# Optimization experiments

Hardware: AMD Instinct MI355X
Metric: run time of the kernel (lower is better)

## Reference

```python
import jax, jax.numpy as jnp
import numpy as np

H = 16          # num_heads
HD = 64         # head_dim = latent_dim // num_heads
RHD = 32        # rope_head_dim = head_dim // 2
NHD = 32        # nope_head_dim
Q_LAT = 256     # latent_dim // compression_ratio
KV_LAT = 204    # xf_latent_dim // (compression_ratio + 1)
MAX_LEN = 2048
THETA = 10000.0
EPS = 1e-5


def _rope_tables():
    half = RHD // 2  # 16
    freqs = 1.0 / THETA ** (np.arange(half, dtype=np.float32) / half)
    t = np.arange(MAX_LEN, dtype=np.float32)
    ang = np.outer(t, freqs)  # (MAX_LEN, half)
    return jnp.asarray(np.cos(ang)), jnp.asarray(np.sin(ang))

COS, SIN = _rope_tables()


def _ln(x, g, b):
    m = jnp.mean(x, axis=-1, keepdims=True)
    v = jnp.var(x, axis=-1, keepdims=True)
    return (x - m) * jax.lax.rsqrt(v + EPS) * g + b


def _rope(t, cos, sin):
    # t: (..., L, RHD); cos/sin: (L, RHD//2); interleaved even/odd convention
    ev, od = t[..., 0::2], t[..., 1::2]
    oe = ev * cos - od * sin
    oo = ev * sin + od * cos
    return jnp.stack([oe, oo], axis=-1).reshape(t.shape)


def setup_inputs() -> dict:
    key = jax.random.key(0)
    ks = jax.random.split(key, 12)
    D = 1024
    s = 0.02
    return {
        "x": jax.random.normal(ks[0], (2, 2048, D), jnp.float32),
        "xf": jax.random.normal(ks[1], (2, 2048, D), jnp.float32),
        "Wqc": jax.random.normal(ks[2], (D, Q_LAT), jnp.float32) * s,
        "gq": jnp.ones((Q_LAT,), jnp.float32),
        "bq": jnp.zeros((Q_LAT,), jnp.float32),
        "Wq_rope": jax.random.normal(ks[3], (Q_LAT, H * RHD), jnp.float32) * s,
        "Wq_nope": jax.random.normal(ks[4], (Q_LAT, H * NHD), jnp.float32) * s,
        "Wkvc": jax.random.normal(ks[5], (D, KV_LAT), jnp.float32) * s,
        "gkv": jnp.ones((KV_LAT,), jnp.float32),
        "bkv": jnp.zeros((KV_LAT,), jnp.float32),
        "Wk_nope": jax.random.normal(ks[6], (KV_LAT, H * NHD), jnp.float32) * s,
        "Wv": jax.random.normal(ks[7], (KV_LAT, H * HD), jnp.float32) * s,
        "Wkr": jax.random.normal(ks[8], (D, RHD), jnp.float32) * s,
        "Wo": jax.random.normal(ks[9], (D, D), jnp.float32) * s,
        "bo": jnp.zeros((D,), jnp.float32),
    }


def reference(x, xf, Wqc, gq, bq, Wq_rope, Wq_nope, Wkvc, gkv, bkv, Wk_nope, Wv, Wkr, Wo, bo):
    B, T, D = x.shape
    S = xf.shape[1]

    # query path: compress -> LN -> decoupled decompress
    ql = _ln(x @ Wqc, gq, bq)                                   # (B,T,Q_LAT)
    q_nope = (ql @ Wq_nope).reshape(B, T, H, NHD).transpose(0, 2, 1, 3)  # (B,H,T,NHD)
    q_rope = (ql @ Wq_rope).reshape(B, T, H, RHD).transpose(0, 2, 1, 3)  # (B,H,T,RHD)

    # key/value path: compress -> LN -> decompress; shared single rope head
    kvl = _ln(xf @ Wkvc, gkv, bkv)                              # (B,S,KV_LAT)
    k_nope = (kvl @ Wk_nope).reshape(B, S, H, NHD).transpose(0, 2, 1, 3)  # (B,H,S,NHD)
    v = (kvl @ Wv).reshape(B, S, H, HD).transpose(0, 2, 1, 3)   # (B,H,S,HD)
    k_rope = (xf @ Wkr).reshape(B, S, 1, RHD).transpose(0, 2, 1, 3)       # (B,1,S,RHD)

    q_rope = _rope(q_rope, COS[:T], SIN[:T])
    k_rope = _rope(k_rope, COS[:S], SIN[:S]) / H
    k_rope = jnp.broadcast_to(k_rope, (B, H, S, RHD))

    q = jnp.concatenate([q_nope, q_rope], axis=-1)              # (B,H,T,HD)
    k = jnp.concatenate([k_nope, k_rope], axis=-1)              # (B,H,S,HD)

    scale = 1.0 / jnp.sqrt(jnp.asarray(HD, q.dtype))
    scores = jnp.einsum("bhtd,bhsd->bhts", q, k) * scale
    attn = jax.nn.softmax(scores, axis=-1)
    o = jnp.einsum("bhts,bhsd->bhtd", attn, v)                  # (B,H,T,HD)
    o = o.transpose(0, 2, 1, 3).reshape(B, T, H * HD)
    return o @ Wo + bo
```

## Files before the change

### kernel.cpp

```cpp
#include <hip/hip_runtime.h>
#include <hip/hip_bf16.h>
#include <math.h>

#define SEQ 2048

typedef __bf16 bf16x8 __attribute__((ext_vector_type(8)));
typedef float  f32x4  __attribute__((ext_vector_type(4)));

#if __has_builtin(__builtin_amdgcn_exp2f)
#define EXP2(x) __builtin_amdgcn_exp2f(x)
#else
#define EXP2(x) exp2f(x)
#endif

__device__ __forceinline__ unsigned short f2bf(float f) {
  __bf16 h = (__bf16)f;
  return __builtin_bit_cast(unsigned short, h);
}

__device__ __forceinline__ void gload16(const unsigned short* g, unsigned short* l) {
  __builtin_amdgcn_global_load_lds(
      (const __attribute__((address_space(1))) void*)g,
      (__attribute__((address_space(3))) void*)l, 16, 0, 0);
}

__device__ __forceinline__ unsigned cvtpk(float lo, float hi) {
  unsigned r;
  asm("v_cvt_pk_bf16_f32 %0, %1, %2" : "=v"(r) : "v"(lo), "v"(hi));
  return r;
}
__device__ __forceinline__ void plswap32(unsigned &a, unsigned &b) {
  asm("v_permlane32_swap_b32 %0, %1" : "+v"(a), "+v"(b));
}
__device__ __forceinline__ void plswap16(unsigned &a, unsigned &b) {
  asm("v_permlane16_swap_b32 %0, %1" : "+v"(a), "+v"(b));
}

#define CLOG (0.125f * 1.44269504f)

struct WPrep {
  const float* src[8];
  unsigned short* dst[8];
  int K[8], N[8], NR[8], KC[8], nb[8];
  float2* cst;
  const float* xs[2];
  unsigned short* xd[2];
};

__global__ __launch_bounds__(256) void wprep_kernel(WPrep p)
{
  __shared__ float tile[32][33];
  int bid = blockIdx.x;
  if (bid < 128) {
    const int idx = bid * 256 + threadIdx.x;
    const int pos = idx >> 4, i = idx & 15;
    const float freq = EXP2(-(float)i * 0.8304820237f);
    const float ang = (float)pos * freq;
    p.cst[idx] = make_float2(cosf(ang), sinf(ang));
    return;
  }
  bid -= 128;
  if (bid < 4096) {
    const int sel = bid >> 11;
    const long base = (long)(bid & 2047) * 2048 + threadIdx.x * 8;
    const float4 a = *(const float4*)&p.xs[sel][base];
    const float4 b = *(const float4*)&p.xs[sel][base + 4];
    ushort4 u0, u1;
    u0.x = f2bf(a.x); u0.y = f2bf(a.y); u0.z = f2bf(a.z); u0.w = f2bf(a.w);
    u1.x = f2bf(b.x); u1.y = f2bf(b.y); u1.z = f2bf(b.z); u1.w = f2bf(b.w);
    *(ushort4*)&p.xd[sel][base] = u0;
    *(ushort4*)&p.xd[sel][base + 4] = u1;
    return;
  }
  bid -= 4096;
  int di = 0;
  while (bid >= p.nb[di]) { bid -= p.nb[di]; ++di; }
  const float* src = p.src[di];
  unsigned short* dst = p.dst[di];
  const int K = p.K[di], N = p.N[di], KC = p.KC[di];
  const int nkx = KC >> 5;
  const int k0 = (bid % nkx) * 32, n0 = (bid / nkx) * 32;
  const int tx = threadIdx.x & 31, ty = threadIdx.x >> 5;
  for (int r = ty; r < 32; r += 8) {
    const int k = k0 + r, n = n0 + tx;
    tile[r][tx] = (k < K && n < N) ? src[(long)k * N + n] : 0.0f;
  }
  __syncthreads();
  for (int r = ty; r < 32; r += 8) {
    const int n = n0 + r, k = k0 + tx;
    dst[(long)n * KC + k] = f2bf(tile[tx][r]);
  }
}

template <int EPI, bool AF32>
__device__ __forceinline__ void gemm_body(
    unsigned short* smem,
    const void* __restrict__ Av, const unsigned short* __restrict__ BT,
    const float* __restrict__ bias, const float2* __restrict__ cst,
    void* __restrict__ C0v, void* __restrict__ C1v, int K, int N,
    int bx, int by)
{
  unsigned short* As = smem;
  unsigned short* Bs = smem + 2 * 128 * 32;
  const int tid = threadIdx.x;
  const int w = tid >> 6, lane = tid & 63;
  const int ln16 = lane & 15, quad = lane >> 4;
  const int wm = (w >> 1) * 64, wn = (w & 1) * 64;
  const int m0 = by * 128, n0 = bx * 128;
  const int rr = tid >> 2, cc = (tid & 3) * 8;

  const unsigned short* A = (const unsigned short*)Av;

  auto stageB = [&](int ib, int k0) {
    gload16(&BT[(long)(n0 + rr)      * K + k0 + cc], &Bs[ib * 4096 + rr * 32 + cc]);
    gload16(&BT[(long)(n0 + 64 + rr) * K + k0 + cc], &Bs[ib * 4096 + (64 + rr) * 32 + cc]);
  };
  auto stageAbf = [&](int ib, int k0) {
    gload16(&A[(long)(m0 + rr)      * K + k0 + cc], &As[ib * 4096 + rr * 32 + cc]);
    gload16(&A[(long)(m0 + 64 + rr) * K + k0 + cc], &As[ib * 4096 + (64 + rr) * 32 + cc]);
  };

  f32x4 acc[4][4];
#pragma unroll
  for (int i = 0; i < 4; ++i)
#pragma unroll
    for (int j = 0; j < 4; ++j)
#pragma unroll
      for (int r = 0; r < 4; ++r) acc[i][j][r] = 0.0f;

  stageB(0, 0);
  stageAbf(0, 0);

  int ib = 0;
  for (int k0 = 0; k0 < K; k0 += 32, ib ^= 1) {
    __syncthreads();
    const int kn = k0 + 32;
    if (kn < K) { stageB(ib ^ 1, kn); stageAbf(ib ^ 1, kn); }
    bf16x8 fa[4], fb[4];
#pragma unroll
    for (int i = 0; i < 4; ++i) fa[i] = *(const bf16x8*)&As[ib * 4096 + (wm + i * 16 + ln16) * 32 + quad * 8];
#pragma unroll
    for (int j = 0; j < 4; ++j) fb[j] = *(const bf16x8*)&Bs[ib * 4096 + (wn + j * 16 + ln16) * 32 + quad * 8];
#pragma unroll
    for (int i = 0; i < 4; ++i)
#pragma unroll
      for (int j = 0; j < 4; ++j)
        acc[i][j] = __builtin_amdgcn_mfma_f32_16x16x32_bf16(fa[i], fb[j], acc[i][j], 0, 0, 0);
  }

  if (EPI == 5 && n0 >= 512) {
    __syncthreads();
#pragma unroll
    for (int i = 0; i < 4; ++i) {
      const int rl = wm + i * 16 + quad * 4;
#pragma unroll
      for (int j = 0; j < 4; ++j) {
        const int cl = wn + j * 16 + ln16;
        ushort4 u;
        u.x = f2bf(acc[i][j][0]); u.y = f2bf(acc[i][j][1]);
        u.z = f2bf(acc[i][j][2]); u.w = f2bf(acc[i][j][3]);
        *(ushort4*)&smem[cl * 132 + rl] = u;
      }
    }
    __syncthreads();
    unsigned short* vT = (unsigned short*)C1v;
    const int b = m0 >> 11, sbase = m0 & (SEQ - 1);
    for (int q = tid; q < 128 * 16; q += 256) {
      const int cl = q >> 4, sch = (q & 15) * 8;
      bf16x8 val = *(const bf16x8*)&smem[cl * 132 + sch];
      const int c = (n0 - 512) + cl;
      const int hh = c >> 6, dd = c & 63;
      *(bf16x8*)&vT[((long)(b * 16 + hh) * 64 + dd) * SEQ + sbase + sch] = val;
    }
    return;
  }
#pragma unroll
  for (int i = 0; i < 4; ++i) {
    const int row0 = m0 + wm + i * 16 + quad * 4;
#pragma unroll
    for (int j = 0; j < 4; ++j) {
      const int col = n0 + wn + j * 16 + ln16;
      if (EPI == 3) {
        if (n0 < 512) {
          unsigned short* qn = (unsigned short*)C0v;
#pragma unroll
          for (int r = 0; r < 4; ++r) qn[(long)(row0 + r) * 512 + col] = f2bf(acc[i][j][r] * CLOG);
        } else {
          unsigned short* qr = (unsigned short*)C1v;
          const int c = col - 512;
          const int d = c & 31;
#pragma unroll
          for (int r = 0; r < 4; ++r) {
            const float v = acc[i][j][r];
            const float p = __shfl_xor(v, 1);
            const float2 t = cst[((row0 + r) & (SEQ - 1)) * 16 + (d >> 1)];
            const float o = ((d & 1) == 0) ? (v * t.x - p * t.y) : (p * t.y + v * t.x);
            qr[(long)(row0 + r) * 512 + c] = f2bf(o * CLOG);
          }
        }
      } else if (EPI == 5) {
        unsigned short* kn = (unsigned short*)C0v;
#pragma unroll
        for (int r = 0; r < 4; ++r) kn[(long)(row0 + r) * 512 + col] = f2bf(acc[i][j][r]);
      }
    }
  }
}

template <int E0, bool AF0, int E1, bool AF1>
__global__ __launch_bounds__(256) void gemm_dual1d(
    const void* __restrict__ A0, const unsigned short* __restrict__ BT0,
    void* __restrict__ C00, void* __restrict__ C01, int K0, int N0, int nx0, int nb0,
    const void* __restrict__ A1, const unsigned short* __restrict__ BT1,
    void* __restrict__ C10, void* __restrict__ C11, int K1, int N1, int nx1,
    const float2* __restrict__ cst)
{
  __shared__ unsigned short smem[16896];
  int bid = blockIdx.x;
  if (bid < nb0) {
    gemm_body<E0, AF0>(smem, A0, BT0, nullptr, cst, C00, C01, K0, N0, bid % nx0, bid / nx0);
  } else {
    bid -= nb0;
    gemm_body<E1, AF1>(smem, A1, BT1, nullptr, cst, C10, C11, K1, N1, bid % nx1, bid / nx1);
  }
}

template <int EPI>
__device__ __forceinline__ void gemm_wbody(
    unsigned short* smem,
    const unsigned short* __restrict__ A, const unsigned short* __restrict__ BT,
    const float* __restrict__ bias, const float2* __restrict__ cst,
    void* __restrict__ C0v, void* __restrict__ C1v, int K, int N,
    int bx, int by)
{
  unsigned short* As = smem;
  unsigned short* Bs = smem + 4096;
  const int tid = threadIdx.x;
  const int w = tid >> 6, lane = tid & 63;
  const int ln16 = lane & 15, quad = lane >> 4;
  const int wm = (w >> 1) * 32, wn = (w & 1) * 64;
  const int m0 = by * 64, n0 = bx * 128;
  const int rr = tid >> 2, cc = (tid & 3) * 8;

  auto stageA = [&](int ib, int k0) {
    gload16(&A[(long)(m0 + rr) * K + k0 + cc], &As[ib * 2048 + rr * 32 + cc]);
  };
  auto stageB = [&](int ib, int k0) {
    gload16(&BT[(long)(n0 + rr)      * K + k0 + cc], &Bs[ib * 4096 + rr * 32 + cc]);
    gload16(&BT[(long)(n0 + 64 + rr) * K + k0 + cc], &Bs[ib * 4096 + (64 + rr) * 32 + cc]);
  };

  f32x4 acc[2][4];
#pragma unroll
  for (int i = 0; i < 2; ++i)
#pragma unroll
    for (int j = 0; j < 4; ++j)
#pragma unroll
      for (int r = 0; r < 4; ++r) acc[i][j][r] = 0.0f;

  stageA(0, 0);
  stageB(0, 0);

  int ib = 0;
  for (int k0 = 0; k0 < K; k0 += 32, ib ^= 1) {
    __syncthreads();
    const int kn = k0 + 32;
    if (kn < K) { stageA(ib ^ 1, kn); stageB(ib ^ 1, kn); }
    bf16x8 fa[2], fb[4];
#pragma unroll
    for (int i = 0; i < 2; ++i) fa[i] = *(const bf16x8*)&As[ib * 2048 + (wm + i * 16 + ln16) * 32 + quad * 8];
#pragma unroll
    for (int j = 0; j < 4; ++j) fb[j] = *(const bf16x8*)&Bs[ib * 4096 + (wn + j * 16 + ln16) * 32 + quad * 8];
#pragma unroll
    for (int i = 0; i < 2; ++i)
#pragma unroll
      for (int j = 0; j < 4; ++j)
        acc[i][j] = __builtin_amdgcn_mfma_f32_16x16x32_bf16(fa[i], fb[j], acc[i][j], 0, 0, 0);
  }

#pragma unroll
  for (int i = 0; i < 2; ++i) {
    const int row0 = m0 + wm + i * 16 + quad * 4;
#pragma unroll
    for (int j = 0; j < 4; ++j) {
      const int col = n0 + wn + j * 16 + ln16;
      if (EPI == 0 || EPI == 1) {
        float* C = (float*)C0v;
        const float bv = (EPI == 1) ? bias[col] : 0.0f;
#pragma unroll
        for (int r = 0; r < 4; ++r) C[(long)(row0 + r) * N + col] = acc[i][j][r] + bv;
      } else if (EPI == 4) {
        if (col < 256) {
          float* kvl = (float*)C0v;
#pragma unroll
          for (int r = 0; r < 4; ++r) kvl[(long)(row0 + r) * 256 + col] = acc[i][j][r];
        } else if (col < 288) {
          unsigned short* kr = (unsigned short*)C1v;
          const int d = col - 256;
#pragma unroll
          for (int r = 0; r < 4; ++r) {
            const float v = acc[i][j][r];
            const float p = __shfl_xor(v, 1);
            const float2 t = cst[((row0 + r) & (SEQ - 1)) * 16 + (d >> 1)];
            const float o = ((d & 1) == 0) ? (v * t.x - p * t.y) : (p * t.y + v * t.x);
            kr[(long)(row0 + r) * 32 + d] = f2bf(o * 0.0625f);
          }
        }
      }
    }
  }
}

template <int EPI>
__global__ __launch_bounds__(256) void gemm_widek(
    const unsigned short* __restrict__ A, const unsigned short* __restrict__ BT,
    const float* __restrict__ bias, const float2* __restrict__ cst,
    void* __restrict__ C0, void* __restrict__ C1, int K, int N)
{
  __shared__ unsigned short smem[12288];
  gemm_wbody<EPI>(smem, A, BT, bias, cst, C0, C1, K, N, blockIdx.x, blockIdx.y);
}

template <int E0, int E1>
__global__ __launch_bounds__(256) void gemm_dualw1d(
    const unsigned short* __restrict__ A0, const unsigned short* __restrict__ BT0,
    void* __restrict__ C00, void* __restrict__ C01, int K0, int N0, int nx0, int nb0,
    const unsigned short* __restrict__ A1, const unsigned short* __restrict__ BT1,
    void* __restrict__ C10, void* __restrict__ C11, int K1, int N1, int nx1,
    const float2* __restrict__ cst)
{
  __shared__ unsigned short smem[12288];
  int bid = blockIdx.x;
  if (bid < nb0) {
    gemm_wbody<E0>(smem, A0, BT0, nullptr, cst, C00, C01, K0, N0, bid % nx0, bid / nx0);
  } else {
    bid -= nb0;
    gemm_wbody<E1>(smem, A1, BT1, nullptr, cst, C10, C11, K1, N1, bid % nx1, bid / nx1);
  }
}

__global__ __launch_bounds__(256) void ln_fast_kernel(
    const float* __restrict__ Xq, const float* __restrict__ Xkv,
    const float* __restrict__ gq, const float* __restrict__ bq,
    const float* __restrict__ gkv, const float* __restrict__ bkv,
    unsigned short* __restrict__ Yq, unsigned short* __restrict__ Ykv)
{
  const int tid = threadIdx.x;
  const int wv = tid >> 6, lane = tid & 63;
  const int row0 = blockIdx.x * 4 + wv;
  const bool isq = row0 < 4096;
  const int row = isq ? row0 : row0 - 4096;
  const float* X = isq ? Xq : Xkv;
  const float* g = isq ? gq : gkv;
  const float* b = isq ? bq : bkv;
  unsigned short* Y = isq ? Yq : Ykv;
  const int C = isq ? 256 : 204;
  const int Cp = isq ? 256 : 224;
  const int col = lane * 4;
  const bool valid = col < C;
  float4 v = make_float4(0.f, 0.f, 0.f, 0.f);
  if (valid) v = *(const float4*)&X[(long)row * 256 + col];
  float s1 = v.x + v.y + v.z + v.w;
  float s2 = v.x * v.x + v.y * v.y + v.z * v.z + v.w * v.w;
#pragma unroll
  for (int off = 1; off < 64; off <<= 1) {
    s1 += __shfl_xor(s1, off);
    s2 += __shfl_xor(s2, off);
  }
  const float mean = s1 / C;
  const float var  = s2 / C - mean * mean;
  const float rs = rsqrtf(var + 1e-5f);
  if (valid) {
    const float4 gv = *(const float4*)&g[col];
    const float4 bv = *(const float4*)&b[col];
    ushort4 u;
    u.x = f2bf((v.x - mean) * rs * gv.x + bv.x);
    u.y = f2bf((v.y - mean) * rs * gv.y + bv.y);
    u.z = f2bf((v.z - mean) * rs * gv.z + bv.z);
    u.w = f2bf((v.w - mean) * rs * gv.w + bv.w);
    *(ushort4*)&Y[(long)row * Cp + col] = u;
  } else if (col < Cp) {
    *(ushort4*)&Y[(long)row * Cp + col] = make_ushort4(0, 0, 0, 0);
  }
}

#define KSTR 36
#define VSTR 68
__global__ __launch_bounds__(256, 2) void attn_mfma_kernel(
    const unsigned short* __restrict__ qn, const unsigned short* __restrict__ qr,
    const unsigned short* __restrict__ kn, const unsigned short* __restrict__ kr,
    const unsigned short* __restrict__ vT, unsigned short* __restrict__ ob)
{
  __shared__ unsigned short Kn[2][64 * KSTR];
  __shared__ unsigned short Vs[2][64 * VSTR];
  const int id = blockIdx.x;
  const int xcd = id & 7, j = id >> 3;
  const int bh = xcd * 4 + (j & 3);
  const int tile = j >> 2;
  const int b = bh >> 4, h = bh & 15;
  const int t0 = tile * 128;
  const int tid = threadIdx.x;
  const int w = tid >> 6, lane = tid & 63;
  const int ln16 = lane & 15, quad = lane >> 4;
  const int trow = w * 16;
  const long bT = (long)b * SEQ;

  const int krow = tid >> 2, kc8 = (tid & 3) * 8;
  const int vd0 = tid >> 3, vc0 = (tid & 7) * 8;
  const int vd1 = vd0 + 32;

  bf16x8 q0A = *(const bf16x8*)&qn[(bT + t0 + trow + ln16) * 512 + h * 32 + quad * 8];
  bf16x8 q1A = *(const bf16x8*)&qr[(bT + t0 + trow + ln16) * 512 + h * 32 + quad * 8];
  bf16x8 q0B = *(const bf16x8*)&qn[(bT + t0 + 64 + trow + ln16) * 512 + h * 32 + quad * 8];
  bf16x8 q1B = *(const bf16x8*)&qr[(bT + t0 + 64 + trow + ln16) * 512 + h * 32 + quad * 8];

  auto loadKV = [&](int s0, bf16x8& rk0, bf16x8& rv0, bf16x8& rv1) {
    rk0 = *(const bf16x8*)&kn[(bT + s0 + krow) * 512 + h * 32 + kc8];
    rv0 = *(const bf16x8*)&vT[((long)bh * 64 + vd0) * SEQ + s0 + vc0];
    rv1 = *(const bf16x8*)&vT[((long)bh * 64 + vd1) * SEQ + s0 + vc0];
  };
  auto writeKV = [&](int ib, bf16x8 rk0, bf16x8 rv0, bf16x8 rv1) {
    *(bf16x8*)&Kn[ib][krow * KSTR + kc8] = rk0;
    *(bf16x8*)&Vs[ib][vd0 * VSTR + vc0] = rv0;
    *(bf16x8*)&Vs[ib][vd1 * VSTR + vc0] = rv1;
  };
  auto loadKrF = [&](int s0, bf16x8* f) {
#pragma unroll
    for (int nt = 0; nt < 4; ++nt)
      f[nt] = *(const bf16x8*)&kr[(bT + s0 + nt * 16 + ln16) * 32 + quad * 8];
  };
  auto pxform = [&](const f32x4* sf, float& l_part, bf16x8& a0, bf16x8& a1) {
    float p[16];
#pragma unroll
    for (int nt = 0; nt < 4; ++nt)
#pragma unroll
      for (int r = 0; r < 4; ++r) {
        const float e = EXP2(sf[nt][r]);
        p[nt * 4 + r] = e;
        l_part += e;
      }
    unsigned u0 = cvtpk(p[0],  p[1]),  u1 = cvtpk(p[2],  p[3]);
    unsigned u2 = cvtpk(p[4],  p[5]),  u3 = cvtpk(p[6],  p[7]);
    unsigned u4 = cvtpk(p[8],  p[9]),  u5 = cvtpk(p[10], p[11]);
    unsigned u6 = cvtpk(p[12], p[13]), u7 = cvtpk(p[14], p[15]);
    plswap32(u0, u2); plswap16(u0, u2);
    plswap32(u1, u3); plswap16(u1, u3);
    plswap32(u4, u6); plswap16(u4, u6);
    plswap32(u5, u7); plswap16(u5, u7);
    const uint4 w0 = make_uint4(u0, u1, u2, u3);
    const uint4 w1 = make_uint4(u4, u5, u6, u7);
    a0 = __builtin_bit_cast(bf16x8, w0);
    a1 = __builtin_bit_cast(bf16x8, w1);
  };

  bf16x8 ck0, cv0, cv1;
  bf16x8 nk0, nv0, nv1;
  bf16x8 ckr[4];
  loadKV(0, ck0, cv0, cv1);
  writeKV(0, ck0, cv0, cv1);
  loadKV(64, nk0, nv0, nv1);
  loadKrF(0, ckr);

  f32x4 o_acc[2][4];
#pragma unroll
  for (int g = 0; g < 2; ++g)
#pragma unroll
    for (int nt = 0; nt < 4; ++nt)
#pragma unroll
      for (int r = 0; r < 4; ++r) o_acc[g][nt][r] = 0.0f;
  float l_part[2] = {0.0f, 0.0f};

  int ib = 0;
  for (int s0 = 0; s0 < SEQ; s0 += 64, ib ^= 1) {
    __syncthreads();
    if (s0 + 64 < SEQ) {
      writeKV(ib ^ 1, nk0, nv0, nv1);
      if (s0 + 128 < SEQ) loadKV(s0 + 128, nk0, nv0, nv1);
    }

    bf16x8 ka[4];
#pragma unroll
    for (int nt = 0; nt < 4; ++nt)
      ka[nt] = *(const bf16x8*)&Kn[ib][(nt * 16 + ln16) * KSTR + quad * 8];

    f32x4 sfA[4], sfB[4];
#pragma unroll
    for (int nt = 0; nt < 4; ++nt)
#pragma unroll
      for (int r = 0; r < 4; ++r) { sfA[nt][r] = 0.0f; sfB[nt][r] = 0.0f; }
#pragma unroll
    for (int nt = 0; nt < 4; ++nt) {
      sfA[nt] = __builtin_amdgcn_mfma_f32_16x16x32_bf16(ka[nt], q0A, sfA[nt], 0, 0, 0);
      sfA[nt] = __builtin_amdgcn_mfma_f32_16x16x32_bf16(ckr[nt], q1A, sfA[nt], 0, 0, 0);
    }
#pragma unroll
    for (int nt = 0; nt < 4; ++nt) {
      sfB[nt] = __builtin_amdgcn_mfma_f32_16x16x32_bf16(ka[nt], q0B, sfB[nt], 0, 0, 0);
      sfB[nt] = __builtin_amdgcn_mfma_f32_16x16x32_bf16(ckr[nt], q1B, sfB[nt], 0, 0, 0);
    }

    if (s0 + 64 < SEQ) loadKrF(s0 + 64, ckr);

    bf16x8 a0A, a1A, a0B, a1B;
    pxform(sfA, l_part[0], a0A, a1A);
    pxform(sfB, l_part[1], a0B, a1B);

#pragma unroll
    for (int nt = 0; nt < 4; ++nt) {
      bf16x8 v0 = *(const bf16x8*)&Vs[ib][(nt * 16 + ln16) * VSTR + quad * 8];
      o_acc[0][nt] = __builtin_amdgcn_mfma_f32_16x16x32_bf16(a0A, v0, o_acc[0][nt], 0, 0, 0);
      o_acc[1][nt] = __builtin_amdgcn_mfma_f32_16x16x32_bf16(a0B, v0, o_acc[1][nt], 0, 0, 0);
      bf16x8 v1 = *(const bf16x8*)&Vs[ib][(nt * 16 + ln16) * VSTR + 32 + quad * 8];
      o_acc[0][nt] = __builtin_amdgcn_mfma_f32_16x16x32_bf16(a1A, v1, o_acc[0][nt], 0, 0, 0);
      o_acc[1][nt] = __builtin_amdgcn_mfma_f32_16x16x32_bf16(a1B, v1, o_acc[1][nt], 0, 0, 0);
    }
  }

#pragma unroll
  for (int g = 0; g < 2; ++g) {
    float l_i = l_part[g];
    l_i += __shfl_xor(l_i, 16);
    l_i += __shfl_xor(l_i, 32);
    const float lr = 1.0f / l_i;
    float lq[4];
#pragma unroll
    for (int r = 0; r < 4; ++r) lq[r] = __shfl(lr, quad * 4 + r);
#pragma unroll
    for (int r = 0; r < 4; ++r) {
      const long t = t0 + g * 64 + trow + quad * 4 + r;
      const long base = (bT + t) * 1024 + h * 64 + ln16;
#pragma unroll
      for (int nt = 0; nt < 4; ++nt)
        ob[base + nt * 16] = f2bf(o_acc[g][nt][r] * lq[r]);
    }
  }
}

extern "C" void kernel_launch(void* const* d_in, const int* in_sizes, int n_in,
                              void* d_out, int out_size, void* d_ws, size_t ws_size,
                              hipStream_t stream) {
  const float* x       = (const float*)d_in[0];
  const float* xf      = (const float*)d_in[1];
  const float* Wqc     = (const float*)d_in[2];
  const float* gq      = (const float*)d_in[3];
  const float* bq      = (const float*)d_in[4];
  const float* Wq_rope = (const float*)d_in[5];
  const float* Wq_nope = (const float*)d_in[6];
  const float* Wkvc    = (const float*)d_in[7];
  const float* gkv     = (const float*)d_in[8];
  const float* bkv     = (const float*)d_in[9];
  const float* Wk_nope = (const float*)d_in[10];
  const float* Wv      = (const float*)d_in[11];
  const float* Wkr     = (const float*)d_in[12];
  const float* Wo      = (const float*)d_in[13];
  const float* bo      = (const float*)d_in[14];
  float* out = (float*)d_out;

  const long R = 4096;
  float* ws = (float*)d_ws;
  float* ql_f  = ws;
  float* kvl_f = ql_f + R * 256;
  float2* cst  = (float2*)(kvl_f + R * 256);
  unsigned short* us = (unsigned short*)(cst + 2048 * 16);
  unsigned short* ql_bf  = us;  us += R * 256;
  unsigned short* kvl_bf = us;  us += R * 224;
  unsigned short* qn_bf  = us;  us += R * 512;
  unsigned short* qr_bf  = us;  us += R * 512;
  unsigned short* kn_bf  = us;  us += R * 512;
  unsigned short* kr_bf  = us;  us += R * 32;
  unsigned short* vT_bf  = us;  us += R * 1024;
  unsigned short* o_bf   = us;  us += R * 1024;
  unsigned short* x_bf   = us;  us += R * 1024;
  unsigned short* xf_bf  = us;  us += R * 1024;
  unsigned short* WqcT   = us;  us += 256 * 1024;
  unsigned short* WkvkrT = us;  us += 384 * 1024;
  unsigned short* WqnqrT = us;  us += 1024 * 256;
  unsigned short* WknvT  = us;  us += 1536 * 224;
  unsigned short* WoT    = us;  us += 1024 * 1024;

  WPrep p;
  const float* srcs[8] = {Wqc, Wkvc, Wkr, Wq_nope, Wq_rope, Wk_nope, Wv, Wo};
  unsigned short* dsts[8] = {WqcT, WkvkrT, WkvkrT + 256 * 1024,
                             WqnqrT, WqnqrT + 512 * 256,
                             WknvT, WknvT + 512 * 224, WoT};
  const int Ks[8]  = {1024, 1024, 1024, 256, 256, 204, 204, 1024};
  const int Ns[8]  = {256, 204, 32, 512, 512, 512, 1024, 1024};
  const int NRs[8] = {256, 256, 128, 512, 512, 512, 1024, 1024};
  const int KCs[8] = {1024, 1024, 1024, 256, 256, 224, 224, 1024};
  int total = 128 + 4096;
  for (int i = 0; i < 8; ++i) {
    p.src[i] = srcs[i]; p.dst[i] = dsts[i];
    p.K[i] = Ks[i]; p.N[i] = Ns[i]; p.NR[i] = NRs[i]; p.KC[i] = KCs[i];
    p.nb[i] = (KCs[i] / 32) * (NRs[i] / 32);
    total += p.nb[i];
  }
  p.cst = cst;
  p.xs[0] = x;  p.xs[1] = xf;
  p.xd[0] = x_bf; p.xd[1] = xf_bf;
  wprep_kernel<<<total, 256, 0, stream>>>(p);

  gemm_dualw1d<0, 4><<<320, 256, 0, stream>>>(
      x_bf, WqcT, ql_f, nullptr, 1024, 256, 2, 128,
      xf_bf, WkvkrT, kvl_f, kr_bf, 1024, 384, 3, cst);
  ln_fast_kernel<<<2048, 256, 0, stream>>>(ql_f, kvl_f, gq, bq, gkv, bkv, ql_bf, kvl_bf);
  gemm_dual1d<3, false, 5, false><<<640, 256, 0, stream>>>(
      ql_bf, WqnqrT, qn_bf, qr_bf, 256, 1024, 8, 256,
      kvl_bf, WknvT, kn_bf, vT_bf, 224, 1536, 12, cst);
  attn_mfma_kernel<<<512, 256, 0, stream>>>(qn_bf, qr_bf, kn_bf, kr_bf, vT_bf, o_bf);
  gemm_widek<1><<<dim3(8, 64), 256, 0, stream>>>(o_bf, WoT, bo, cst, out, nullptr, 1024, 1024);
}
```

Before: 208.3 us.

## Enlarge attention block to 256 query rows with 8 waves sharing K/V tiles

The attention kernel now runs 512 threads per block and covers 256 query rows, up from 256 threads and 128 rows, so the grid shrinks to 256 blocks. Each K/V tile staged in shared memory is reused by 8 waves instead of 4. This halves the global and LDS staging traffic per query row, and K/V loading is spread over more threads. In exchange, each barrier now waits on twice as many waves, and there is one block per CU instead of two, so less independent work can hide stalls.

```diff
diff --git a/kernel.cpp b/kernel.cpp
--- a/kernel.cpp
+++ b/kernel.cpp
@@ -386,7 +386,7 @@
 
 #define KSTR 36
 #define VSTR 68
-__global__ __launch_bounds__(256, 2) void attn_mfma_kernel(
+__global__ __launch_bounds__(512, 1) void attn_mfma_kernel(
     const unsigned short* __restrict__ qn, const unsigned short* __restrict__ qr,
     const unsigned short* __restrict__ kn, const unsigned short* __restrict__ kr,
     const unsigned short* __restrict__ vT, unsigned short* __restrict__ ob)
@@ -398,31 +398,28 @@
   const int bh = xcd * 4 + (j & 3);
   const int tile = j >> 2;
   const int b = bh >> 4, h = bh & 15;
-  const int t0 = tile * 128;
+  const int t0 = tile * 256;
   const int tid = threadIdx.x;
   const int w = tid >> 6, lane = tid & 63;
   const int ln16 = lane & 15, quad = lane >> 4;
   const int trow = w * 16;
   const long bT = (long)b * SEQ;
 
+  const int vdr = tid >> 3, vcc = (tid & 7) * 8;
   const int krow = tid >> 2, kc8 = (tid & 3) * 8;
-  const int vd0 = tid >> 3, vc0 = (tid & 7) * 8;
-  const int vd1 = vd0 + 32;
 
   bf16x8 q0A = *(const bf16x8*)&qn[(bT + t0 + trow + ln16) * 512 + h * 32 + quad * 8];
   bf16x8 q1A = *(const bf16x8*)&qr[(bT + t0 + trow + ln16) * 512 + h * 32 + quad * 8];
-  bf16x8 q0B = *(const bf16x8*)&qn[(bT + t0 + 64 + trow + ln16) * 512 + h * 32 + quad * 8];
-  bf16x8 q1B = *(const bf16x8*)&qr[(bT + t0 + 64 + trow + ln16) * 512 + h * 32 + quad * 8];
-
-  auto loadKV = [&](int s0, bf16x8& rk0, bf16x8& rv0, bf16x8& rv1) {
-    rk0 = *(const bf16x8*)&kn[(bT + s0 + krow) * 512 + h * 32 + kc8];
-    rv0 = *(const bf16x8*)&vT[((long)bh * 64 + vd0) * SEQ + s0 + vc0];
-    rv1 = *(const bf16x8*)&vT[((long)bh * 64 + vd1) * SEQ + s0 + vc0];
-  };
-  auto writeKV = [&](int ib, bf16x8 rk0, bf16x8 rv0, bf16x8 rv1) {
-    *(bf16x8*)&Kn[ib][krow * KSTR + kc8] = rk0;
-    *(bf16x8*)&Vs[ib][vd0 * VSTR + vc0] = rv0;
-    *(bf16x8*)&Vs[ib][vd1 * VSTR + vc0] = rv1;
+  bf16x8 q0B = *(const bf16x8*)&qn[(bT + t0 + 128 + trow + ln16) * 512 + h * 32 + quad * 8];
+  bf16x8 q1B = *(const bf16x8*)&qr[(bT + t0 + 128 + trow + ln16) * 512 + h * 32 + quad * 8];
+
+  auto loadKV = [&](int s0, bf16x8& rk, bf16x8& rv) {
+    rv = *(const bf16x8*)&vT[((long)bh * 64 + vdr) * SEQ + s0 + vcc];
+    if (tid < 256) rk = *(const bf16x8*)&kn[(bT + s0 + krow) * 512 + h * 32 + kc8];
+  };
+  auto writeKV = [&](int ib, bf16x8 rk, bf16x8 rv) {
+    *(bf16x8*)&Vs[ib][vdr * VSTR + vcc] = rv;
+    if (tid < 256) *(bf16x8*)&Kn[ib][krow * KSTR + kc8] = rk;
   };
   auto loadKrF = [&](int s0, bf16x8* f) {
 #pragma unroll
@@ -453,12 +450,12 @@
     a1 = __builtin_bit_cast(bf16x8, w1);
   };
 
-  bf16x8 ck0, cv0, cv1;
-  bf16x8 nk0, nv0, nv1;
+  bf16x8 ck, cv;
+  bf16x8 nk, nv;
   bf16x8 ckr[4];
-  loadKV(0, ck0, cv0, cv1);
-  writeKV(0, ck0, cv0, cv1);
-  loadKV(64, nk0, nv0, nv1);
+  loadKV(0, ck, cv);
+  writeKV(0, ck, cv);
+  loadKV(64, nk, nv);
   loadKrF(0, ckr);
 
   f32x4 o_acc[2][4];
@@ -474,8 +471,8 @@
   for (int s0 = 0; s0 < SEQ; s0 += 64, ib ^= 1) {
     __syncthreads();
     if (s0 + 64 < SEQ) {
-      writeKV(ib ^ 1, nk0, nv0, nv1);
-      if (s0 + 128 < SEQ) loadKV(s0 + 128, nk0, nv0, nv1);
+      writeKV(ib ^ 1, nk, nv);
+      if (s0 + 128 < SEQ) loadKV(s0 + 128, nk, nv);
     }
 
     bf16x8 ka[4];
@@ -527,7 +524,7 @@
     for (int r = 0; r < 4; ++r) lq[r] = __shfl(lr, quad * 4 + r);
 #pragma unroll
     for (int r = 0; r < 4; ++r) {
-      const long t = t0 + g * 64 + trow + quad * 4 + r;
+      const long t = t0 + g * 128 + trow + quad * 4 + r;
       const long base = (bT + t) * 1024 + h * 64 + ln16;
 #pragma unroll
       for (int nt = 0; nt < 4; ++nt)
@@ -606,6 +603,6 @@
   gemm_dual1d<3, false, 5, false><<<640, 256, 0, stream>>>(
       ql_bf, WqnqrT, qn_bf, qr_bf, 256, 1024, 8, 256,
       kvl_bf, WknvT, kn_bf, vT_bf, 224, 1536, 12, cst);
-  attn_mfma_kernel<<<512, 256, 0, stream>>>(qn_bf, qr_bf, kn_bf, kr_bf, vT_bf, o_bf);
+  attn_mfma_kernel<<<256, 512, 0, stream>>>(qn_bf, qr_bf, kn_bf, kr_bf, vT_bf, o_bf);
   gemm_widek<1><<<dim3(8, 64), 256, 0, stream>>>(o_bf, WoT, bo, cst, out, nullptr, 1024, 1024);
 }
```

Measured after the change: 208.3 us. Within noise of the previous version (-0.0%).
